# Kernel tuning notes

Hardware: AMD Instinct MI355X
Metric: run time of the kernel (lower is better)

## Reference

```python
import jax, jax.numpy as jnp
import numpy as np

N = 50000      # nodes
E = 800000     # edges (avg degree 16)
G = 64         # graphs in batch


def gcn_conv(x, edge_index, W, b):
    """PyG GCNConv: h = D^{-1/2}(A+I)D^{-1/2} (x @ W) + b, self-loops added."""
    n = x.shape[0]
    h = x @ W  # [N, out]
    loop = jnp.arange(n, dtype=edge_index.dtype)
    src = jnp.concatenate([edge_index[0], loop])
    dst = jnp.concatenate([edge_index[1], loop])
    deg = jax.ops.segment_sum(jnp.ones_like(dst, dtype=h.dtype), dst, num_segments=n)
    dinv = jnp.where(deg > 0, jax.lax.rsqrt(deg), 0.0)
    norm = dinv[src] * dinv[dst]               # [E+N]
    msg = h[src] * norm[:, None]               # gather + scale
    return jax.ops.segment_sum(msg, dst, num_segments=n) + b


def setup_inputs() -> dict:
    key = jax.random.key(0)
    ks = jax.random.split(key, 12)
    x = jax.random.normal(ks[0], (N, 512), dtype=jnp.float32)
    edge_index = jax.random.randint(ks[1], (2, E), 0, N, dtype=jnp.int64)
    batch = jnp.sort(jax.random.randint(ks[2], (N,), 0, G, dtype=jnp.int64))

    def lin(k, fin, fout):
        s = 1.0 / np.sqrt(fin)
        return jax.random.uniform(k, (fin, fout), jnp.float32, -s, s)

    return {
        "x": x, "edge_index": edge_index, "batch": batch,
        "W1": lin(ks[3], 512, 256), "b1": jnp.zeros((256,), jnp.float32),
        "W2": lin(ks[4], 256, 128), "b2": jnp.zeros((128,), jnp.float32),
        "W3": lin(ks[5], 128, 64),  "b3": jnp.zeros((64,), jnp.float32),
        "Wl": lin(ks[6], 64, 2),    "bl": jnp.zeros((2,), jnp.float32),
    }


def reference(x, edge_index, batch, W1, b1, W2, b2, W3, b3, Wl, bl):
    h = jax.nn.relu(gcn_conv(x, edge_index, W1, b1))
    h = jax.nn.relu(gcn_conv(h, edge_index, W2, b2))
    h = gcn_conv(h, edge_index, W3, b3)
    # global_mean_pool over batch ids
    sums = jax.ops.segment_sum(h, batch, num_segments=G)
    cnts = jax.ops.segment_sum(jnp.ones((h.shape[0],), h.dtype), batch, num_segments=G)
    pooled = sums / jnp.maximum(cnts, 1.0)[:, None]
    # dropout p=0.5 is identity in eval mode
    return pooled @ Wl + bl  # [G, 2]
```

## Files before the change

kernel.cpp:

```cpp
#include <hip/hip_runtime.h>
#include <hip/hip_bf16.h>


typedef __attribute__((ext_vector_type(8))) short short8_t;
typedef __attribute__((ext_vector_type(4))) float float4_t;

__device__ __forceinline__ unsigned short f2bf(float f) {
    unsigned int u = __float_as_uint(f);
    u += 0x7FFFu + ((u >> 16) & 1u);
    return (unsigned short)(u >> 16);
}
__device__ __forceinline__ float bf2f(unsigned short h) {
    return __uint_as_float(((unsigned int)h) << 16);
}

#define GLDS16(gp, lp)                                                          \
    __builtin_amdgcn_global_load_lds(                                           \
        (const __attribute__((address_space(1))) void*)(gp),                    \
        (__attribute__((address_space(3))) void*)(lp), 16, 0, 0)


__global__ __launch_bounds__(256) void prep(const float* __restrict__ x,
                                            ushort* __restrict__ Xb,
                                            const float* __restrict__ W1, ushort* __restrict__ Wt1,
                                            const float* __restrict__ W2, ushort* __restrict__ Wt2,
                                            const float* __restrict__ W3, ushort* __restrict__ Wt3,
                                            int* __restrict__ zbase,
                                            int M, int Mpad, int nzero, int nxblk) {
    int bx = blockIdx.x;
    if (bx < nxblk) {
        int t = bx * 256 + threadIdx.x;
        int row = t >> 7;
        ushort4 o;
        if (row < M) {
            float4 v = ((const float4*)x)[t];
            o.x = f2bf(v.x); o.y = f2bf(v.y); o.z = f2bf(v.z); o.w = f2bf(v.w);
        } else {
            o.x = o.y = o.z = o.w = 0;
        }
        if (row < Mpad) ((ushort4*)Xb)[t] = o;
    } else if (bx < nxblk + 704) {
        int t = (bx - nxblk) * 256 + threadIdx.x;
        if (t < 131072) {
            int k = t & 511, n = t >> 9;
            Wt1[t] = f2bf(W1[(size_t)k * 256 + n]);
        } else if (t < 163840) {
            int u = t - 131072;
            int k = u & 255, n = u >> 8;
            Wt2[u] = f2bf(W2[(size_t)k * 128 + n]);
        } else if (t < 180224) {
            int u = t - 163840;
            int k = u & 127, n = u >> 7;
            Wt3[u] = (n < 64) ? f2bf(W3[(size_t)k * 64 + n]) : (ushort)0;
        }
    } else {
        int t = (bx - nxblk - 704) * 256 + threadIdx.x;
        if (t < nzero) zbase[t] = 0;
    }
}


__global__ void count_indeg(const int* __restrict__ dst, int* __restrict__ indeg, int E) {
    int e = blockIdx.x * blockDim.x + threadIdx.x;
    if (e < E) atomicAdd(&indeg[dst[e]], 1);
}

__global__ __launch_bounds__(1024) void scan1(const int* __restrict__ indeg,
                                              int* __restrict__ incl,
                                              int* __restrict__ part, int n) {
    __shared__ int sm[1024];
    int i = blockIdx.x * 1024 + threadIdx.x;
    int v = (i < n) ? indeg[i] : 0;
    sm[threadIdx.x] = v;
    __syncthreads();
    #pragma unroll
    for (int off = 1; off < 1024; off <<= 1) {
        int t = (threadIdx.x >= (unsigned)off) ? sm[threadIdx.x - off] : 0;
        __syncthreads();
        sm[threadIdx.x] += t;
        __syncthreads();
    }
    if (i < n) incl[i] = sm[threadIdx.x];
    if (threadIdx.x == 1023) part[blockIdx.x] = sm[1023];
}

__global__ __launch_bounds__(256) void scan23(const int* __restrict__ indeg,
                                              int* __restrict__ rowptr,
                                              int* __restrict__ cursor,
                                              const int* __restrict__ part,
                                              float* __restrict__ dinv,
                                              int n, int npad, int E, int nb) {
    __shared__ int ps[64];
    int tid = threadIdx.x;
    if (tid < 64) {
        int v = (tid < nb) ? part[tid] : 0;
        int orig = v;
        #pragma unroll
        for (int off = 1; off < 64; off <<= 1) {
            int u = __shfl_up(v, off, 64);
            if (tid >= off) v += u;
        }
        ps[tid] = v - orig;
    }
    __syncthreads();
    int i = blockIdx.x * 256 + tid;
    if (i < n) {
        int excl = rowptr[i] - indeg[i] + ps[i >> 10];
        rowptr[i] = excl;
        cursor[i] = excl;
        dinv[i] = rsqrtf((float)indeg[i] + 1.0f);
    } else if (i < npad) {
        dinv[i] = 0.f;
    }
    if (i == 0) rowptr[n] = E;
}

__global__ void fill_csr(const int* __restrict__ src, const int* __restrict__ dst,
                         int* __restrict__ cursor, int* __restrict__ col, int E) {
    int e = blockIdx.x * blockDim.x + threadIdx.x;
    if (e < E) {
        int p = atomicAdd(&cursor[dst[e]], 1);
        col[p] = src[e];
    }
}


__device__ __forceinline__ void mfma_step(const ushort* __restrict__ Asb,
                                          const ushort* __restrict__ Bsb,
                                          int arow, int brow, int quad,
                                          float4_t (&acc)[4][4]) {
    short8_t aF[4], bF[4];
    #pragma unroll
    for (int i = 0; i < 4; ++i)
        aF[i] = *(const short8_t*)&Asb[(arow + i * 16) * 32 + quad * 8];
    #pragma unroll
    for (int j = 0; j < 4; ++j)
        bF[j] = *(const short8_t*)&Bsb[(brow + j * 16) * 32 + quad * 8];
    #pragma unroll
    for (int i = 0; i < 4; ++i)
        #pragma unroll
        for (int j = 0; j < 4; ++j)
            acc[i][j] = __builtin_amdgcn_mfma_f32_16x16x32_bf16(aF[i], bF[j], acc[i][j], 0, 0, 0);
}

__global__ __launch_bounds__(256) void gemm_mfma(const ushort* __restrict__ A,
                                                 const ushort* __restrict__ Bt,
                                                 const float* __restrict__ dinv,
                                                 ushort* __restrict__ C,
                                                 int Ncols, int K, int ldc) {
    __shared__ __align__(16) ushort As[2 * 4096];
    __shared__ __align__(16) ushort Bs[2 * 4096];
    int tid = threadIdx.x;
    int lane = tid & 63, w = tid >> 6;
    int wr = w >> 1, wc = w & 1;
    int bm = blockIdx.x * 128, bn = blockIdx.y * 128;

    float4_t acc[4][4];
    #pragma unroll
    for (int i = 0; i < 4; ++i)
        #pragma unroll
        for (int j = 0; j < 4; ++j) acc[i][j] = (float4_t)0.0f;

    int r0 = tid >> 2;
    int kb = (tid & 3) * 8;
    const ushort* ga0 = A + (size_t)(bm + r0) * K + kb;
    const ushort* ga1 = A + (size_t)(bm + r0 + 64) * K + kb;
    const ushort* gb0 = Bt + (size_t)(bn + r0) * K + kb;
    const ushort* gb1 = Bt + (size_t)(bn + r0 + 64) * K + kb;
    int w512 = w * 512;

#define ISSUE_DMA(kk, bufofs)                              \
    do {                                                   \
        GLDS16(ga0 + (kk), As + (bufofs) + w512);          \
        GLDS16(ga1 + (kk), As + (bufofs) + 2048 + w512);   \
        GLDS16(gb0 + (kk), Bs + (bufofs) + w512);          \
        GLDS16(gb1 + (kk), Bs + (bufofs) + 2048 + w512);   \
    } while (0)

    int arow = wr * 64 + (lane & 15);
    int brow = wc * 64 + (lane & 15);
    int quad = lane >> 4;

    ISSUE_DMA(0, 0);
    for (int k0 = 0; k0 < K; k0 += 64) {
        __syncthreads();
        ISSUE_DMA(k0 + 32, 4096);
        mfma_step(As, Bs, arow, brow, quad, acc);
        __syncthreads();
        if (k0 + 64 < K) ISSUE_DMA(k0 + 64, 0);
        mfma_step(As + 4096, Bs + 4096, arow, brow, quad, acc);
    }
#undef ISSUE_DMA

    int colb = bn + wc * 64 + (lane & 15);
    #pragma unroll
    for (int i = 0; i < 4; ++i) {
        int mb = bm + wr * 64 + i * 16 + quad * 4;
        #pragma unroll
        for (int r = 0; r < 4; ++r) {
            int m = mb + r;
            float s = dinv[m];
            #pragma unroll
            for (int j = 0; j < 4; ++j) {
                int n = colb + j * 16;
                if (n < Ncols) C[(size_t)m * ldc + n] = f2bf(acc[i][j][r] * s);
            }
        }
    }
}


template <int DW> struct VecT;
template <> struct VecT<2> { using type = uint2; };
template <> struct VecT<4> { using type = uint4; };

template <int F, bool RELU>
__global__ __launch_bounds__(256) void agg_bf(const ushort* __restrict__ g,
                                              const int* __restrict__ rowptr,
                                              const int* __restrict__ col,
                                              const float* __restrict__ dinv,
                                              const float* __restrict__ bias,
                                              ushort* __restrict__ out,
                                              int n, int npad, int zrow) {
    constexpr int EPL  = (F == 64) ? 4 : 2;
    constexpr int SUBW = 64 / EPL;
    constexpr int EPT  = F / SUBW;
    constexpr int LPG  = 16 / EPL;
    constexpr int DW   = EPT / 2;
    using vec_t = typename VecT<DW>::type;

    int wid = (int)((blockIdx.x * blockDim.x + threadIdx.x) >> 6);
    int lane = threadIdx.x & 63;
    if (wid >= npad) return;
    int h   = lane / SUBW;
    int sub = lane & (SUBW - 1);
    int off = sub * EPT;
    ushort* orow = out + (size_t)wid * F + off;

    if (wid >= n) {
        if (h == 0) {
            #pragma unroll
            for (int d = 0; d < DW; ++d) ((uint*)orow)[d] = 0;
        }
        return;
    }

    const ushort* gofs = g + off;
    vec_t sv = *(const vec_t*)(gofs + (size_t)wid * F);
    float self[EPT];
    #pragma unroll
    for (int d = 0; d < DW; ++d) {
        uint dw = ((const uint*)&sv)[d];
        self[2 * d]     = __uint_as_float(dw << 16);
        self[2 * d + 1] = __uint_as_float(dw & 0xffff0000u);
    }

    float acc[EPT];
    #pragma unroll
    for (int t = 0; t < EPT; ++t) acc[t] = 0.f;

    int e0 = rowptr[wid];
    int deg = rowptr[wid + 1] - e0;

    for (int base = 0; base < deg; base += 64) {
        int cnt = min(64, deg - base);
        int ec = (lane < cnt) ? col[e0 + base + lane] : zrow;
        for (int j = 0; j < cnt; j += 16) {
            vec_t v[LPG];
            #pragma unroll
            for (int u = 0; u < LPG; ++u) {
                int id = __shfl(ec, j + u * EPL + h);
                v[u] = *(const vec_t*)(gofs + (size_t)id * F);
            }
            #pragma unroll
            for (int u = 0; u < LPG; ++u)
                #pragma unroll
                for (int d = 0; d < DW; ++d) {
                    uint dw = ((const uint*)&v[u])[d];
                    acc[2 * d]     += __uint_as_float(dw << 16);
                    acc[2 * d + 1] += __uint_as_float(dw & 0xffff0000u);
                }
        }
    }

    #pragma unroll
    for (int t = 0; t < EPT; ++t) {
        if constexpr (EPL == 4) acc[t] += __shfl_xor(acc[t], 16, 64);
        acc[t] += __shfl_xor(acc[t], 32, 64);
    }

    float di = dinv[wid];
    ushort res[EPT];
    #pragma unroll
    for (int t = 0; t < EPT; ++t) {
        float r = di * (acc[t] + self[t]) + bias[off + t];
        if (RELU) r = fmaxf(r, 0.f);
        res[t] = f2bf(r);
    }
    if (h == 0) {
        #pragma unroll
        for (int d = 0; d < DW; ++d)
            ((uint*)orow)[d] = (uint)res[2 * d] | ((uint)res[2 * d + 1] << 16);
    }
}


__global__ __launch_bounds__(256) void pool_sorted(const ushort* __restrict__ h,
                                                   const int* __restrict__ batch,
                                                   float* __restrict__ sums,
                                                   float* __restrict__ cnt, int n) {
    int wave = (int)((blockIdx.x * blockDim.x + threadIdx.x) >> 6);
    int lane = threadIdx.x & 63;
    int start = wave * 64;
    if (start >= n) return;
    int end = min(start + 64, n);
    float acc = 0.f;
    int cur = batch[start];
    int runlen = 0;
    for (int i = start; i < end; ++i) {
        int b = batch[i];
        if (b != cur) {
            atomicAdd(&sums[cur * 64 + lane], acc);
            if (lane == 0) atomicAdd(&cnt[cur], (float)runlen);
            acc = 0.f;
            runlen = 0;
            cur = b;
        }
        acc += bf2f(h[(size_t)i * 64 + lane]);
        runlen++;
    }
    atomicAdd(&sums[cur * 64 + lane], acc);
    if (lane == 0) atomicAdd(&cnt[cur], (float)runlen);
}

__global__ void final_lin(const float* __restrict__ sums, const float* __restrict__ cnt,
                          const float* __restrict__ Wl, const float* __restrict__ bl,
                          float* __restrict__ out) {
    int t = threadIdx.x;
    int g = t >> 1, j = t & 1;
    float c = fmaxf(cnt[g], 1.0f);
    float a = 0.f;
    #pragma unroll
    for (int k = 0; k < 64; ++k) a += sums[g * 64 + k] * Wl[k * 2 + j];
    out[t] = a / c + bl[j];
}


extern "C" void kernel_launch(void* const* d_in, const int* in_sizes, int n_in,
                              void* d_out, int out_size, void* d_ws, size_t ws_size,
                              hipStream_t stream) {
    const float* x   = (const float*)d_in[0];
    const int*   ei  = (const int*)d_in[1];
    const int*   bat = (const int*)d_in[2];
    const float* W1  = (const float*)d_in[3];
    const float* b1  = (const float*)d_in[4];
    const float* W2  = (const float*)d_in[5];
    const float* b2  = (const float*)d_in[6];
    const float* W3  = (const float*)d_in[7];
    const float* b3  = (const float*)d_in[8];
    const float* Wl  = (const float*)d_in[9];
    const float* bl  = (const float*)d_in[10];
    float* out = (float*)d_out;

    const int N = in_sizes[0] / 512;
    const int E = in_sizes[1] / 2;
    const int Mpad = ((N + 127) / 128) * 128;
    const int* src = ei;
    const int* dst = ei + E;

    char* w = (char*)d_ws;
    auto alloc = [&](size_t bytes) {
        char* p = w;
        w += (bytes + 255) & ~(size_t)255;
        return p;
    };
    ushort* Xb   = (ushort*)alloc((size_t)Mpad * 512 * 2);
    ushort* G    = (ushort*)alloc((size_t)Mpad * 256 * 2);
    ushort* H    = (ushort*)alloc((size_t)Mpad * 256 * 2);
    ushort* Wt1  = (ushort*)alloc(256 * 512 * 2);
    ushort* Wt2  = (ushort*)alloc(128 * 256 * 2);
    ushort* Wt3  = (ushort*)alloc(128 * 128 * 2);
    float* dinv  = (float*)alloc((size_t)Mpad * 4);
    int* rowptr  = (int*)alloc((size_t)(N + 1) * 4);
    int* cursor  = (int*)alloc((size_t)N * 4);
    int* col     = (int*)alloc((size_t)(E + 16) * 4);
    int* part    = (int*)alloc(256 * 4);
    int nzero = N + 64 * 64 + 64;
    int* indeg   = (int*)alloc((size_t)nzero * 4);
    float* sums  = (float*)(indeg + N);
    float* cnt   = sums + 64 * 64;

    int nxblk = (Mpad * 128 + 255) / 256;
    int nzblk = (nzero + 255) / 256;
    prep<<<nxblk + 704 + nzblk, 256, 0, stream>>>(x, Xb, W1, Wt1, W2, Wt2, W3, Wt3,
                                                  indeg, N, Mpad, nzero, nxblk);

    count_indeg<<<(E + 255) / 256, 256, 0, stream>>>(dst, indeg, E);
    int nb = (N + 1023) / 1024;
    scan1<<<nb, 1024, 0, stream>>>(indeg, rowptr, part, N);
    scan23<<<(Mpad + 255) / 256, 256, 0, stream>>>(indeg, rowptr, cursor, part, dinv,
                                                   N, Mpad, E, nb);
    fill_csr<<<(E + 255) / 256, 256, 0, stream>>>(src, dst, cursor, col, E);

    int npad = Mpad;
    gemm_mfma<<<dim3(Mpad / 128, 2), 256, 0, stream>>>(Xb, Wt1, dinv, G, 256, 512, 256);
    agg_bf<256, true><<<npad / 4, 256, 0, stream>>>(G, rowptr, col, dinv, b1, H, N, npad, N);
    gemm_mfma<<<dim3(Mpad / 128, 1), 256, 0, stream>>>(H, Wt2, dinv, G, 128, 256, 128);
    agg_bf<128, true><<<npad / 4, 256, 0, stream>>>(G, rowptr, col, dinv, b2, H, N, npad, N);
    gemm_mfma<<<dim3(Mpad / 128, 1), 256, 0, stream>>>(H, Wt3, dinv, G, 64, 128, 64);
    agg_bf<64, false><<<npad / 4, 256, 0, stream>>>(G, rowptr, col, dinv, b3, H, N, npad, N);

    pool_sorted<<<(N + 255) / 256, 256, 0, stream>>>(H, bat, sums, cnt, N);
    final_lin<<<1, 128, 0, stream>>>(sums, cnt, Wl, bl, out);
}
```

Before: 473.2 us.

## Fuse aggregation with next-layer GEMM and merge CSR build into prep/GEMM launches

Replaces the separate aggregate and GEMM kernels for layers 1→2 and 2→3 with one agg_gemm kernel. It aggregates 128 rows into LDS, applies bias and ReLU, then multiplies by the next weight matrix with MFMA, so the intermediate H tensor is never written to or read back from global memory. The in-degree counting moves into the prep kernel, and the CSR fill is merged into the first GEMM launch as extra blocks, which cuts the number of kernel launches. The cost is that each agg_gemm block handles 128 rows with only 8 waves, giving less parallelism for the latency-bound gather. Placing the atomic fill inside the GEMM launch may also contend with the MFMA blocks.

```diff
diff --git a/kernel.cpp b/kernel.cpp
--- a/kernel.cpp
+++ b/kernel.cpp
@@ -1,5 +1,4 @@
 #include <hip/hip_runtime.h>
-#include <hip/hip_bf16.h>
 
 
 typedef __attribute__((ext_vector_type(8))) short short8_t;
@@ -19,14 +18,22 @@
         (const __attribute__((address_space(1))) void*)(gp),                    \
         (__attribute__((address_space(3))) void*)(lp), 16, 0, 0)
 
+template <int DWN> struct VecT;
+template <> struct VecT<2> { using type = uint2; };
+template <> struct VecT<4> { using type = uint4; };
+
+__global__ void zero_k(int* __restrict__ p, int n) {
+    int i = blockIdx.x * blockDim.x + threadIdx.x;
+    if (i < n) p[i] = 0;
+}
 
 __global__ __launch_bounds__(256) void prep(const float* __restrict__ x,
                                             ushort* __restrict__ Xb,
                                             const float* __restrict__ W1, ushort* __restrict__ Wt1,
                                             const float* __restrict__ W2, ushort* __restrict__ Wt2,
                                             const float* __restrict__ W3, ushort* __restrict__ Wt3,
-                                            int* __restrict__ zbase,
-                                            int M, int Mpad, int nzero, int nxblk) {
+                                            const int* __restrict__ dst, int* __restrict__ indeg,
+                                            int M, int Mpad, int E, int nxblk) {
     int bx = blockIdx.x;
     if (bx < nxblk) {
         int t = bx * 256 + threadIdx.x;
@@ -39,30 +46,24 @@
             o.x = o.y = o.z = o.w = 0;
         }
         if (row < Mpad) ((ushort4*)Xb)[t] = o;
-    } else if (bx < nxblk + 704) {
+    } else if (bx < nxblk + 672) {
         int t = (bx - nxblk) * 256 + threadIdx.x;
         if (t < 131072) {
-            int k = t & 511, n = t >> 9;
-            Wt1[t] = f2bf(W1[(size_t)k * 256 + n]);
+            int k = t & 511, nn = t >> 9;
+            Wt1[t] = f2bf(W1[(size_t)k * 256 + nn]);
         } else if (t < 163840) {
             int u = t - 131072;
-            int k = u & 255, n = u >> 8;
-            Wt2[u] = f2bf(W2[(size_t)k * 128 + n]);
-        } else if (t < 180224) {
+            int k = u & 255, nn = u >> 8;
+            Wt2[u] = f2bf(W2[(size_t)k * 128 + nn]);
+        } else {
             int u = t - 163840;
-            int k = u & 127, n = u >> 7;
-            Wt3[u] = (n < 64) ? f2bf(W3[(size_t)k * 64 + n]) : (ushort)0;
+            int k = u & 127, nn = u >> 7;
+            Wt3[u] = f2bf(W3[(size_t)k * 64 + nn]);
         }
     } else {
-        int t = (bx - nxblk - 704) * 256 + threadIdx.x;
-        if (t < nzero) zbase[t] = 0;
-    }
-}
-
-
-__global__ void count_indeg(const int* __restrict__ dst, int* __restrict__ indeg, int E) {
-    int e = blockIdx.x * blockDim.x + threadIdx.x;
-    if (e < E) atomicAdd(&indeg[dst[e]], 1);
+        int t = (bx - nxblk - 672) * 256 + threadIdx.x;
+        if (t < E) atomicAdd(&indeg[dst[t]], 1);
+    }
 }
 
 __global__ __launch_bounds__(1024) void scan1(const int* __restrict__ indeg,
@@ -115,45 +116,31 @@
     if (i == 0) rowptr[n] = E;
 }
 
-__global__ void fill_csr(const int* __restrict__ src, const int* __restrict__ dst,
-                         int* __restrict__ cursor, int* __restrict__ col, int E) {
-    int e = blockIdx.x * blockDim.x + threadIdx.x;
-    if (e < E) {
-        int p = atomicAdd(&cursor[dst[e]], 1);
-        col[p] = src[e];
-    }
-}
-
-
-__device__ __forceinline__ void mfma_step(const ushort* __restrict__ Asb,
-                                          const ushort* __restrict__ Bsb,
-                                          int arow, int brow, int quad,
-                                          float4_t (&acc)[4][4]) {
-    short8_t aF[4], bF[4];
-    #pragma unroll
-    for (int i = 0; i < 4; ++i)
-        aF[i] = *(const short8_t*)&Asb[(arow + i * 16) * 32 + quad * 8];
-    #pragma unroll
-    for (int j = 0; j < 4; ++j)
-        bF[j] = *(const short8_t*)&Bsb[(brow + j * 16) * 32 + quad * 8];
-    #pragma unroll
-    for (int i = 0; i < 4; ++i)
-        #pragma unroll
-        for (int j = 0; j < 4; ++j)
-            acc[i][j] = __builtin_amdgcn_mfma_f32_16x16x32_bf16(aF[i], bF[j], acc[i][j], 0, 0, 0);
-}
-
-__global__ __launch_bounds__(256) void gemm_mfma(const ushort* __restrict__ A,
-                                                 const ushort* __restrict__ Bt,
-                                                 const float* __restrict__ dinv,
-                                                 ushort* __restrict__ C,
-                                                 int Ncols, int K, int ldc) {
+__global__ __launch_bounds__(256) void gemm1_fill(const ushort* __restrict__ A,
+                                                  const ushort* __restrict__ Bt,
+                                                  const float* __restrict__ dinv,
+                                                  ushort* __restrict__ C,
+                                                  const int* __restrict__ src,
+                                                  const int* __restrict__ dst,
+                                                  int* __restrict__ cursor,
+                                                  int* __restrict__ colx,
+                                                  int E, int ngemm) {
     __shared__ __align__(16) ushort As[2 * 4096];
     __shared__ __align__(16) ushort Bs[2 * 4096];
+    int bx = blockIdx.x;
+    if (bx >= ngemm) {
+        int e = (bx - ngemm) * 256 + threadIdx.x;
+        if (e < E) {
+            int p = atomicAdd(&cursor[dst[e]], 1);
+            colx[p] = src[e];
+        }
+        return;
+    }
+    constexpr int K = 512;
     int tid = threadIdx.x;
     int lane = tid & 63, w = tid >> 6;
     int wr = w >> 1, wc = w & 1;
-    int bm = blockIdx.x * 128, bn = blockIdx.y * 128;
+    int bm = (bx >> 1) * 128, bn = (bx & 1) * 128;
 
     float4_t acc[4][4];
     #pragma unroll
@@ -185,10 +172,36 @@
     for (int k0 = 0; k0 < K; k0 += 64) {
         __syncthreads();
         ISSUE_DMA(k0 + 32, 4096);
-        mfma_step(As, Bs, arow, brow, quad, acc);
+        {
+            short8_t aF[4], bF[4];
+            #pragma unroll
+            for (int i = 0; i < 4; ++i)
+                aF[i] = *(const short8_t*)&As[(arow + i * 16) * 32 + quad * 8];
+            #pragma unroll
+            for (int j = 0; j < 4; ++j)
+                bF[j] = *(const short8_t*)&Bs[(brow + j * 16) * 32 + quad * 8];
+            #pragma unroll
+            for (int i = 0; i < 4; ++i)
+                #pragma unroll
+                for (int j = 0; j < 4; ++j)
+                    acc[i][j] = __builtin_amdgcn_mfma_f32_16x16x32_bf16(aF[i], bF[j], acc[i][j], 0, 0, 0);
+        }
         __syncthreads();
         if (k0 + 64 < K) ISSUE_DMA(k0 + 64, 0);
-        mfma_step(As + 4096, Bs + 4096, arow, brow, quad, acc);
+        {
+            short8_t aF[4], bF[4];
+            #pragma unroll
+            for (int i = 0; i < 4; ++i)
+                aF[i] = *(const short8_t*)&As[4096 + (arow + i * 16) * 32 + quad * 8];
+            #pragma unroll
+            for (int j = 0; j < 4; ++j)
+                bF[j] = *(const short8_t*)&Bs[4096 + (brow + j * 16) * 32 + quad * 8];
+            #pragma unroll
+            for (int i = 0; i < 4; ++i)
+                #pragma unroll
+                for (int j = 0; j < 4; ++j)
+                    acc[i][j] = __builtin_amdgcn_mfma_f32_16x16x32_bf16(aF[i], bF[j], acc[i][j], 0, 0, 0);
+        }
     }
 #undef ISSUE_DMA
 
@@ -203,16 +216,140 @@
             #pragma unroll
             for (int j = 0; j < 4; ++j) {
                 int n = colb + j * 16;
-                if (n < Ncols) C[(size_t)m * ldc + n] = f2bf(acc[i][j][r] * s);
+                C[(size_t)m * 256 + n] = f2bf(acc[i][j][r] * s);
             }
         }
     }
 }
 
-
-template <int DW> struct VecT;
-template <> struct VecT<2> { using type = uint2; };
-template <> struct VecT<4> { using type = uint4; };
+template <int FIN, int NOUT>
+__global__ __launch_bounds__(512) void agg_gemm(const ushort* __restrict__ g,
+                                                const int* __restrict__ rowptr,
+                                                const int* __restrict__ col,
+                                                const float* __restrict__ dinv,
+                                                const float* __restrict__ bias,
+                                                const ushort* __restrict__ Bt,
+                                                ushort* __restrict__ C,
+                                                int n, int zrow) {
+    constexpr int NCH = FIN / 32;
+    constexpr int EPT = FIN / 32;
+    constexpr int DWN = EPT / 2;
+    using vec_t = typename VecT<DWN>::type;
+    __shared__ __align__(16) ushort As[NCH * 128 * 32];
+
+    int tid = threadIdx.x;
+    int lane = tid & 63, wv = tid >> 6;
+    int bm = blockIdx.x * 128;
+    int h = lane >> 5, sub = lane & 31;
+    int off = sub * EPT;
+    const ushort* gofs = g + off;
+    int cch0 = off >> 5, kk0 = off & 31;
+
+    for (int q = 0; q < 16; ++q) {
+        int r = wv * 16 + q;
+        int m = bm + r;
+        ushort* ap = As + cch0 * 4096 + r * 32 + kk0;
+        if (m >= n) {
+            if (h == 0) {
+                #pragma unroll
+                for (int d = 0; d < DWN; ++d) ((uint*)ap)[d] = 0;
+            }
+            continue;
+        }
+        vec_t sv = *(const vec_t*)(gofs + (size_t)m * FIN);
+        float self[EPT], acc[EPT];
+        #pragma unroll
+        for (int d = 0; d < DWN; ++d) {
+            uint dw = ((const uint*)&sv)[d];
+            self[2 * d]     = __uint_as_float(dw << 16);
+            self[2 * d + 1] = __uint_as_float(dw & 0xffff0000u);
+        }
+        #pragma unroll
+        for (int t = 0; t < EPT; ++t) acc[t] = 0.f;
+
+        int e0 = rowptr[m];
+        int deg = rowptr[m + 1] - e0;
+        for (int base = 0; base < deg; base += 64) {
+            int cnt = min(64, deg - base);
+            int ec = (lane < cnt) ? col[e0 + base + lane] : zrow;
+            for (int j = 0; j < cnt; j += 16) {
+                vec_t v[8];
+                #pragma unroll
+                for (int u = 0; u < 8; ++u) {
+                    int id = __shfl(ec, j + u * 2 + h);
+                    v[u] = *(const vec_t*)(gofs + (size_t)id * FIN);
+                }
+                #pragma unroll
+                for (int u = 0; u < 8; ++u)
+                    #pragma unroll
+                    for (int d = 0; d < DWN; ++d) {
+                        uint dw = ((const uint*)&v[u])[d];
+                        acc[2 * d]     += __uint_as_float(dw << 16);
+                        acc[2 * d + 1] += __uint_as_float(dw & 0xffff0000u);
+                    }
+            }
+        }
+        #pragma unroll
+        for (int t = 0; t < EPT; ++t) acc[t] += __shfl_xor(acc[t], 32, 64);
+
+        if (h == 0) {
+            float di = dinv[m];
+            uint pk[DWN];
+            #pragma unroll
+            for (int d = 0; d < DWN; ++d) {
+                float r0 = fmaxf(di * (acc[2 * d]     + self[2 * d])     + bias[off + 2 * d],     0.f);
+                float r1 = fmaxf(di * (acc[2 * d + 1] + self[2 * d + 1]) + bias[off + 2 * d + 1], 0.f);
+                pk[d] = (uint)f2bf(r0) | ((uint)f2bf(r1) << 16);
+            }
+            #pragma unroll
+            for (int d = 0; d < DWN; ++d) ((uint*)ap)[d] = pk[d];
+        }
+    }
+    __syncthreads();
+
+    constexpr int WC = NOUT / 32;
+    constexpr int WR = 8 / WC;
+    constexpr int MI = 8 / WR;
+    int wr = wv / WC, wc = wv % WC;
+    int quad = lane >> 4, l15 = lane & 15;
+    float4_t acc2[MI][2];
+    #pragma unroll
+    for (int i = 0; i < MI; ++i) {
+        acc2[i][0] = (float4_t)0.f;
+        acc2[i][1] = (float4_t)0.f;
+    }
+    int arowb = wr * (MI * 16) + l15;
+    const ushort* bp = Bt + (size_t)(wc * 32 + l15) * FIN + quad * 8;
+    #pragma unroll
+    for (int c = 0; c < NCH; ++c) {
+        short8_t aF[MI], bF[2];
+        #pragma unroll
+        for (int i = 0; i < MI; ++i)
+            aF[i] = *(const short8_t*)&As[c * 4096 + (arowb + i * 16) * 32 + quad * 8];
+        #pragma unroll
+        for (int j = 0; j < 2; ++j)
+            bF[j] = *(const short8_t*)(bp + (size_t)(j * 16) * FIN + c * 32);
+        #pragma unroll
+        for (int i = 0; i < MI; ++i) {
+            acc2[i][0] = __builtin_amdgcn_mfma_f32_16x16x32_bf16(aF[i], bF[0], acc2[i][0], 0, 0, 0);
+            acc2[i][1] = __builtin_amdgcn_mfma_f32_16x16x32_bf16(aF[i], bF[1], acc2[i][1], 0, 0, 0);
+        }
+    }
+    #pragma unroll
+    for (int i = 0; i < MI; ++i) {
+        int mb = bm + wr * (MI * 16) + i * 16 + quad * 4;
+        #pragma unroll
+        for (int rr = 0; rr < 4; ++rr) {
+            int m = mb + rr;
+            float s = dinv[m];
+            #pragma unroll
+            for (int j = 0; j < 2; ++j) {
+                int ncol = wc * 32 + j * 16 + l15;
+                C[(size_t)m * NOUT + ncol] = f2bf(acc2[i][j][rr] * s);
+            }
+        }
+    }
+}
 
 template <int F, bool RELU>
 __global__ __launch_bounds__(256) void agg_bf(const ushort* __restrict__ g,
@@ -226,8 +363,8 @@
     constexpr int SUBW = 64 / EPL;
     constexpr int EPT  = F / SUBW;
     constexpr int LPG  = 16 / EPL;
-    constexpr int DW   = EPT / 2;
-    using vec_t = typename VecT<DW>::type;
+    constexpr int DWN  = EPT / 2;
+    using vec_t = typename VecT<DWN>::type;
 
     int wid = (int)((blockIdx.x * blockDim.x + threadIdx.x) >> 6);
     int lane = threadIdx.x & 63;
@@ -240,7 +377,7 @@
     if (wid >= n) {
         if (h == 0) {
             #pragma unroll
-            for (int d = 0; d < DW; ++d) ((uint*)orow)[d] = 0;
+            for (int d = 0; d < DWN; ++d) ((uint*)orow)[d] = 0;
         }
         return;
     }
@@ -249,7 +386,7 @@
     vec_t sv = *(const vec_t*)(gofs + (size_t)wid * F);
     float self[EPT];
     #pragma unroll
-    for (int d = 0; d < DW; ++d) {
+    for (int d = 0; d < DWN; ++d) {
         uint dw = ((const uint*)&sv)[d];
         self[2 * d]     = __uint_as_float(dw << 16);
         self[2 * d + 1] = __uint_as_float(dw & 0xffff0000u);
@@ -275,7 +412,7 @@
             #pragma unroll
             for (int u = 0; u < LPG; ++u)
                 #pragma unroll
-                for (int d = 0; d < DW; ++d) {
+                for (int d = 0; d < DWN; ++d) {
                     uint dw = ((const uint*)&v[u])[d];
                     acc[2 * d]     += __uint_as_float(dw << 16);
                     acc[2 * d + 1] += __uint_as_float(dw & 0xffff0000u);
@@ -299,7 +436,7 @@
     }
     if (h == 0) {
         #pragma unroll
-        for (int d = 0; d < DW; ++d)
+        for (int d = 0; d < DWN; ++d)
             ((uint*)orow)[d] = (uint)res[2 * d] | ((uint)res[2 * d + 1] << 16);
     }
 }
@@ -375,11 +512,13 @@
         return p;
     };
     ushort* Xb   = (ushort*)alloc((size_t)Mpad * 512 * 2);
-    ushort* G    = (ushort*)alloc((size_t)Mpad * 256 * 2);
-    ushort* H    = (ushort*)alloc((size_t)Mpad * 256 * 2);
+    ushort* G1   = (ushort*)alloc((size_t)Mpad * 256 * 2);
+    ushort* G2   = (ushort*)alloc((size_t)Mpad * 128 * 2);
+    ushort* G3   = (ushort*)alloc((size_t)Mpad * 64 * 2);
+    ushort* H3   = (ushort*)alloc((size_t)Mpad * 64 * 2);
     ushort* Wt1  = (ushort*)alloc(256 * 512 * 2);
     ushort* Wt2  = (ushort*)alloc(128 * 256 * 2);
-    ushort* Wt3  = (ushort*)alloc(128 * 128 * 2);
+    ushort* Wt3  = (ushort*)alloc(64 * 128 * 2);
     float* dinv  = (float*)alloc((size_t)Mpad * 4);
     int* rowptr  = (int*)alloc((size_t)(N + 1) * 4);
     int* cursor  = (int*)alloc((size_t)N * 4);
@@ -390,26 +529,29 @@
     float* sums  = (float*)(indeg + N);
     float* cnt   = sums + 64 * 64;
 
+    zero_k<<<(nzero + 255) / 256, 256, 0, stream>>>(indeg, nzero);
+
     int nxblk = (Mpad * 128 + 255) / 256;
-    int nzblk = (nzero + 255) / 256;
-    prep<<<nxblk + 704 + nzblk, 256, 0, stream>>>(x, Xb, W1, Wt1, W2, Wt2, W3, Wt3,
-                                                  indeg, N, Mpad, nzero, nxblk);
-
-    count_indeg<<<(E + 255) / 256, 256, 0, stream>>>(dst, indeg, E);
+    int ncblk = (E + 255) / 256;
+    prep<<<nxblk + 672 + ncblk, 256, 0, stream>>>(x, Xb, W1, Wt1, W2, Wt2, W3, Wt3,
+                                                  dst, indeg, N, Mpad, E, nxblk);
+
     int nb = (N + 1023) / 1024;
     scan1<<<nb, 1024, 0, stream>>>(indeg, rowptr, part, N);
     scan23<<<(Mpad + 255) / 256, 256, 0, stream>>>(indeg, rowptr, cursor, part, dinv,
                                                    N, Mpad, E, nb);
-    fill_csr<<<(E + 255) / 256, 256, 0, stream>>>(src, dst, cursor, col, E);
-
-    int npad = Mpad;
-    gemm_mfma<<<dim3(Mpad / 128, 2), 256, 0, stream>>>(Xb, Wt1, dinv, G, 256, 512, 256);
-    agg_bf<256, true><<<npad / 4, 256, 0, stream>>>(G, rowptr, col, dinv, b1, H, N, npad, N);
-    gemm_mfma<<<dim3(Mpad / 128, 1), 256, 0, stream>>>(H, Wt2, dinv, G, 128, 256, 128);
-    agg_bf<128, true><<<npad / 4, 256, 0, stream>>>(G, rowptr, col, dinv, b2, H, N, npad, N);
-    gemm_mfma<<<dim3(Mpad / 128, 1), 256, 0, stream>>>(H, Wt3, dinv, G, 64, 128, 64);
-    agg_bf<64, false><<<npad / 4, 256, 0, stream>>>(G, rowptr, col, dinv, b3, H, N, npad, N);
-
-    pool_sorted<<<(N + 255) / 256, 256, 0, stream>>>(H, bat, sums, cnt, N);
+
+    int ngemm = (Mpad / 128) * 2;
+    gemm1_fill<<<ngemm + ncblk, 256, 0, stream>>>(Xb, Wt1, dinv, G1, src, dst,
+                                                  cursor, col, E, ngemm);
+
+    agg_gemm<256, 128><<<Mpad / 128, 512, 0, stream>>>(G1, rowptr, col, dinv, b1,
+                                                       Wt2, G2, N, N);
+    agg_gemm<128, 64><<<Mpad / 128, 512, 0, stream>>>(G2, rowptr, col, dinv, b2,
+                                                      Wt3, G3, N, N);
+    agg_bf<64, false><<<Mpad / 4, 256, 0, stream>>>(G3, rowptr, col, dinv, b3, H3,
+                                                    N, Mpad, N);
+
+    pool_sorted<<<(N + 255) / 256, 256, 0, stream>>>(H3, bat, sums, cnt, N);
     final_lin<<<1, 128, 0, stream>>>(sums, cnt, Wl, bl, out);
 }
```

New measurement: 443.5 us. -6.3%, faster.
